# Kernel optimization log

Hardware: AMD Instinct MI355X
Metric: run time of the kernel (lower is better)

## Reference

```python
import jax, jax.numpy as jnp
import numpy as np

N = 50000          # nodes
E = 800000         # edges
F_IN, H, OUT = 512, 256, 2
BN_EPS = 1e-5


def setup_inputs() -> dict:
    key = jax.random.key(0)
    ks = jax.random.split(key, 10)
    x = jax.random.normal(ks[0], (N, F_IN), jnp.float32)
    edge_index = jax.random.randint(ks[1], (2, E), 0, N, dtype=jnp.int64)
    edge_weight = jax.random.uniform(ks[2], (E,), jnp.float32)

    def lin(k, fan_in, fan_out):
        return jax.random.normal(k, (fan_in, fan_out), jnp.float32) / np.sqrt(fan_in).astype(np.float32)

    W1, b1 = lin(ks[3], F_IN, H), jnp.zeros((H,), jnp.float32)
    W2, b2 = lin(ks[4], H, H), jnp.zeros((H,), jnp.float32)
    W3, b3 = lin(ks[5], H, OUT), jnp.zeros((OUT,), jnp.float32)
    # BatchNorm1d affine params + running stats (eval mode)
    g1, be1 = jnp.ones((H,), jnp.float32), jnp.zeros((H,), jnp.float32)
    m1 = 0.1 * jax.random.normal(ks[6], (H,), jnp.float32)
    v1 = jax.random.uniform(ks[7], (H,), jnp.float32, 0.5, 1.5)
    g2, be2 = jnp.ones((H,), jnp.float32), jnp.zeros((H,), jnp.float32)
    m2 = 0.1 * jax.random.normal(ks[8], (H,), jnp.float32)
    v2 = jax.random.uniform(ks[9], (H,), jnp.float32, 0.5, 1.5)
    return {"x": x, "edge_index": edge_index, "edge_weight": edge_weight,
            "W1": W1, "b1": b1, "g1": g1, "be1": be1, "m1": m1, "v1": v1,
            "W2": W2, "b2": b2, "g2": g2, "be2": be2, "m2": m2, "v2": v2,
            "W3": W3, "b3": b3}


def gcn_conv(x, row, col, w, W, b):
    # PyG GCNConv (eval): h = x @ W; out[col] += norm * h[row]; + b
    # row/col/w already include self-loops with weight 1.
    n = x.shape[0]
    h = x @ W                                      # [N, out]
    deg = jax.ops.segment_sum(w, col, num_segments=n)
    dinv = jnp.where(deg > 0, jax.lax.rsqrt(deg), 0.0)
    norm = dinv[row] * w * dinv[col]               # [E+N]
    out = jax.ops.segment_sum(h[row] * norm[:, None], col, num_segments=n)
    return out + b


def batchnorm_eval(x, g, be, m, v):
    return (x - m) * jax.lax.rsqrt(v + BN_EPS) * g + be


def reference(x, edge_index, edge_weight, W1, b1, g1, be1, m1, v1,
              W2, b2, g2, be2, m2, v2, W3, b3):
    n = x.shape[0]
    loops = jnp.arange(n, dtype=edge_index.dtype)
    row = jnp.concatenate([edge_index[0], loops])
    col = jnp.concatenate([edge_index[1], loops])
    w = jnp.concatenate([edge_weight, jnp.ones((n,), x.dtype)])

    h = jax.nn.relu(batchnorm_eval(gcn_conv(x, row, col, w, W1, b1), g1, be1, m1, v1))
    h = jax.nn.relu(batchnorm_eval(gcn_conv(h, row, col, w, W2, b2), g2, be2, m2, v2))
    return gcn_conv(h, row, col, w, W3, b3)
```

## Files before the change

kernel.cpp:

```cpp
#include <hip/hip_runtime.h>
#include <stdint.h>

#define F_IN 512
#define HF 256
#define OUT_F 2
#define BN_EPS 1e-5f
#define SCAN_B 256
#define LDSTR 36

typedef __attribute__((ext_vector_type(8))) short bf16x8;
typedef __attribute__((ext_vector_type(4))) float f32x4;

__device__ inline float bf2f(unsigned short u) {
    union { float f; uint32_t i; } v; v.i = ((uint32_t)u) << 16; return v.f;
}
__device__ inline unsigned short f2bf(float f) {
    union { float f; uint32_t i; } v; v.f = f;
    uint32_t r = v.i + 0x7FFFu + ((v.i >> 16) & 1u);
    return (unsigned short)(r >> 16);
}

__global__ void prep_kernel(unsigned long long* __restrict__ packed,
                            const float* __restrict__ W1, unsigned short* __restrict__ W1t,
                            const float* __restrict__ W2, unsigned short* __restrict__ W2t,
                            unsigned short* __restrict__ xbf_pad,
                            unsigned short* __restrict__ bufa_pad,
                            int n, int padx, int pada) {
    int idx = blockIdx.x * blockDim.x + threadIdx.x;
    if (idx < n) { packed[idx] = 1ULL << 20; return; }
    int j = idx - n;
    if (j < F_IN * HF) {
        int nn = j >> 9, k = j & (F_IN - 1);
        W1t[j] = f2bf(W1[(size_t)k * HF + nn]);
        return;
    }
    j -= F_IN * HF;
    if (j < HF * HF) {
        int nn = j >> 8, k = j & (HF - 1);
        W2t[j] = f2bf(W2[(size_t)k * HF + nn]);
        return;
    }
    j -= HF * HF;
    if (j < padx) { xbf_pad[j] = 0; return; }
    j -= padx;
    if (j < pada) bufa_pad[j] = 0;
}

__global__ void count_conv_kernel(const int* __restrict__ col,
                                  const float* __restrict__ w,
                                  unsigned long long* __restrict__ packed,
                                  const float* __restrict__ x,
                                  unsigned short* __restrict__ xbf,
                                  int e, int nchunk) {
    int tid = blockIdx.x * blockDim.x + threadIdx.x;
    int base = blockIdx.x * 1024 + (int)threadIdx.x;
    #pragma unroll
    for (int k = 0; k < 4; ++k) {
        int i = base + k * 256;
        if (i < e) {
            unsigned long long add = (1ULL << 40)
                | (unsigned long long)__float2uint_rn(w[i] * 1048576.0f);
            atomicAdd(&packed[col[i]], add);
        }
    }
    const int stride = gridDim.x * blockDim.x;
    const float4* x4 = (const float4*)x;
    for (int c = tid; c < nchunk; c += stride) {
        float4 f0 = x4[2 * c];
        float4 f1 = x4[2 * c + 1];
        bf16x8 v;
        v[0] = (short)f2bf(f0.x); v[1] = (short)f2bf(f0.y);
        v[2] = (short)f2bf(f0.z); v[3] = (short)f2bf(f0.w);
        v[4] = (short)f2bf(f1.x); v[5] = (short)f2bf(f1.y);
        v[6] = (short)f2bf(f1.z); v[7] = (short)f2bf(f1.w);
        *(bf16x8*)(xbf + (size_t)c * 8) = v;
    }
}

__global__ __launch_bounds__(256)
void gemm_kernel(const unsigned short* __restrict__ A,
                 const unsigned short* __restrict__ Bt,
                 unsigned short* __restrict__ C, int K) {
    __shared__ unsigned short As[2][128 * LDSTR];
    __shared__ unsigned short Bs[2][128 * LDSTR];
    const int tid  = threadIdx.x;
    const int lane = tid & 63;
    const int wv   = tid >> 6;
    const int wrow = wv >> 1, wcol = wv & 1;
    const int m0 = blockIdx.x * 128;
    const int n0 = blockIdx.y * 128;

    const int sr = tid >> 2;
    const int sc = (tid & 3) * 8;

    const unsigned short* pa0 = A + (size_t)(m0 + sr) * K + sc;
    const unsigned short* pa1 = A + (size_t)(m0 + sr + 64) * K + sc;
    const unsigned short* pb0 = Bt + (size_t)(n0 + sr) * K + sc;
    const unsigned short* pb1 = Bt + (size_t)(n0 + sr + 64) * K + sc;

    f32x4 zero4 = {0.0f, 0.0f, 0.0f, 0.0f};
    f32x4 acc[4][4];
    #pragma unroll
    for (int i = 0; i < 4; ++i)
        #pragma unroll
        for (int j = 0; j < 4; ++j) acc[i][j] = zero4;

    const int q8 = (lane >> 4) * 8;
    const int ml = lane & 15;

    bf16x8 va0 = *(const bf16x8*)pa0;
    bf16x8 va1 = *(const bf16x8*)pa1;
    bf16x8 vb0 = *(const bf16x8*)pb0;
    bf16x8 vb1 = *(const bf16x8*)pb1;

    const int nsteps = K >> 5;
    for (int s = 0; s < nsteps; ++s) {
        const int buf = s & 1;
        *(bf16x8*)&As[buf][sr * LDSTR + sc]        = va0;
        *(bf16x8*)&As[buf][(sr + 64) * LDSTR + sc] = va1;
        *(bf16x8*)&Bs[buf][sr * LDSTR + sc]        = vb0;
        *(bf16x8*)&Bs[buf][(sr + 64) * LDSTR + sc] = vb1;
        __syncthreads();
        if (s + 1 < nsteps) {
            int off = (s + 1) * 32;
            va0 = *(const bf16x8*)(pa0 + off);
            va1 = *(const bf16x8*)(pa1 + off);
            vb0 = *(const bf16x8*)(pb0 + off);
            vb1 = *(const bf16x8*)(pb1 + off);
        }
        bf16x8 af[4], bfr[4];
        #pragma unroll
        for (int i = 0; i < 4; ++i)
            af[i] = *(const bf16x8*)&As[buf][(wrow * 64 + i * 16 + ml) * LDSTR + q8];
        #pragma unroll
        for (int j = 0; j < 4; ++j)
            bfr[j] = *(const bf16x8*)&Bs[buf][(wcol * 64 + j * 16 + ml) * LDSTR + q8];
        #pragma unroll
        for (int i = 0; i < 4; ++i)
            #pragma unroll
            for (int j = 0; j < 4; ++j)
                acc[i][j] = __builtin_amdgcn_mfma_f32_16x16x32_bf16(af[i], bfr[j], acc[i][j], 0, 0, 0);
    }

    const int q4 = (lane >> 4) * 4;
    #pragma unroll
    for (int i = 0; i < 4; ++i) {
        #pragma unroll
        for (int j = 0; j < 4; ++j) {
            #pragma unroll
            for (int rg = 0; rg < 4; ++rg) {
                int r = m0 + wrow * 64 + i * 16 + q4 + rg;
                int c = n0 + wcol * 64 + j * 16 + ml;
                C[(size_t)r * HF + c] = f2bf(acc[i][j][rg]);
            }
        }
    }
}

__global__ void scan1_kernel(const unsigned long long* __restrict__ packed,
                             int* __restrict__ local, int* __restrict__ blocksum, int n) {
    __shared__ int tmp[SCAN_B];
    int i = blockIdx.x * SCAN_B + threadIdx.x;
    int v = (i < n) ? (int)(packed[i] >> 40) : 0;
    tmp[threadIdx.x] = v;
    __syncthreads();
    for (int off = 1; off < SCAN_B; off <<= 1) {
        int t = 0;
        if ((int)threadIdx.x >= off) t = tmp[threadIdx.x - off];
        __syncthreads();
        if ((int)threadIdx.x >= off) tmp[threadIdx.x] += t;
        __syncthreads();
    }
    if (i < n) local[i] = tmp[threadIdx.x] - v;
    if (threadIdx.x == SCAN_B - 1) blocksum[blockIdx.x] = tmp[SCAN_B - 1];
}

__global__ void scan3_dinv_kernel(int* __restrict__ csr_ptr, int* __restrict__ cursor,
                                  const int* __restrict__ blocksum,
                                  const unsigned long long* __restrict__ packed,
                                  float* __restrict__ dinv, int n, int e, int nb) {
    __shared__ int red[SCAN_B];
    int t = threadIdx.x;
    red[t] = (t < nb && t < (int)blockIdx.x) ? blocksum[t] : 0;
    __syncthreads();
    for (int off = SCAN_B / 2; off > 0; off >>= 1) {
        if (t < off) red[t] += red[t + off];
        __syncthreads();
    }
    int prefix = red[0];
    int i = blockIdx.x * SCAN_B + t;
    if (i < n) {
        int val = csr_ptr[i] + prefix;
        csr_ptr[i] = val;
        cursor[i] = val;
        float deg = (float)(packed[i] & 0xFFFFFFFFFFULL) * (1.0f / 1048576.0f);
        dinv[i] = rsqrtf(deg);
    }
    if (i == 0) csr_ptr[n] = e;
}

__global__ void fill_kernel(const int* __restrict__ row, const int* __restrict__ col,
                            const float* __restrict__ w, const float* __restrict__ dinv,
                            int* __restrict__ cursor, int2* __restrict__ csr_edge, int e) {
    int i = blockIdx.x * blockDim.x + threadIdx.x;
    if (i < e) {
        int r = row[i], c = col[i];
        int pos = atomicAdd(&cursor[c], 1);
        float nrm = dinv[r] * w[i] * dinv[c];
        csr_edge[pos] = make_int2(r, __float_as_int(nrm));
    }
}

template<int FINAL>
__global__ void agg_kernel(const unsigned short* __restrict__ h,
                           const int* __restrict__ ptr,
                           const int2* __restrict__ edge,
                           const float* __restrict__ dinv,
                           const float* __restrict__ b, const float* __restrict__ g,
                           const float* __restrict__ be, const float* __restrict__ m,
                           const float* __restrict__ v,
                           unsigned short* __restrict__ out,
                           const float* __restrict__ W3, float* __restrict__ h3, int n) {
    int wid  = (blockIdx.x * blockDim.x + threadIdx.x) >> 6;
    int lane = threadIdx.x & 63;
    if (wid >= n) return;
    int p0 = ptr[wid], p1 = ptr[wid + 1];
    const int fo = lane * 4;
    float a0 = 0.f, a1 = 0.f, a2 = 0.f, a3 = 0.f;

    const int pend = p0 + ((p1 - p0) & ~7);
    for (int p = p0; p < pend; p += 8) {
        int2 ed[8];
        #pragma unroll
        for (int k = 0; k < 8; ++k) ed[k] = edge[p + k];
        ushort4 hv[8];
        #pragma unroll
        for (int k = 0; k < 8; ++k)
            hv[k] = *(const ushort4*)(h + (size_t)ed[k].x * HF + fo);
        #pragma unroll
        for (int k = 0; k < 8; ++k) {
            float nw = __int_as_float(ed[k].y);
            a0 += nw * bf2f(hv[k].x);
            a1 += nw * bf2f(hv[k].y);
            a2 += nw * bf2f(hv[k].z);
            a3 += nw * bf2f(hv[k].w);
        }
    }
    if (pend < p1) {
        int2 ed[8];
        float wv[8];
        #pragma unroll
        for (int k = 0; k < 8; ++k) {
            int idx = pend + k < p1 ? pend + k : p1 - 1;
            ed[k] = edge[idx];
            wv[k] = (pend + k < p1) ? __int_as_float(ed[k].y) : 0.0f;
        }
        ushort4 hv[8];
        #pragma unroll
        for (int k = 0; k < 8; ++k)
            hv[k] = *(const ushort4*)(h + (size_t)ed[k].x * HF + fo);
        #pragma unroll
        for (int k = 0; k < 8; ++k) {
            a0 += wv[k] * bf2f(hv[k].x);
            a1 += wv[k] * bf2f(hv[k].y);
            a2 += wv[k] * bf2f(hv[k].z);
            a3 += wv[k] * bf2f(hv[k].w);
        }
    }
    float s = dinv[wid];
    float sl = s * s;
    ushort4 hv = *(const ushort4*)(h + (size_t)wid * HF + fo);
    a0 += sl * bf2f(hv.x);
    a1 += sl * bf2f(hv.y);
    a2 += sl * bf2f(hv.z);
    a3 += sl * bf2f(hv.w);

    float4 bb  = *(const float4*)(b + fo);
    float4 gg  = *(const float4*)(g + fo);
    float4 bee = *(const float4*)(be + fo);
    float4 mm  = *(const float4*)(m + fo);
    float4 vv  = *(const float4*)(v + fo);
    float f0 = fmaxf((a0 + bb.x - mm.x) * rsqrtf(vv.x + BN_EPS) * gg.x + bee.x, 0.f);
    float f1 = fmaxf((a1 + bb.y - mm.y) * rsqrtf(vv.y + BN_EPS) * gg.y + bee.y, 0.f);
    float f2 = fmaxf((a2 + bb.z - mm.z) * rsqrtf(vv.z + BN_EPS) * gg.z + bee.z, 0.f);
    float f3 = fmaxf((a3 + bb.w - mm.w) * rsqrtf(vv.w + BN_EPS) * gg.w + bee.w, 0.f);

    if (!FINAL) {
        ushort4 o;
        o.x = f2bf(f0); o.y = f2bf(f1); o.z = f2bf(f2); o.w = f2bf(f3);
        *(ushort4*)(out + (size_t)wid * HF + fo) = o;
    } else {
        float4 w0 = *(const float4*)(W3 + fo * 2);
        float4 w1 = *(const float4*)(W3 + fo * 2 + 4);
        float s0 = f0 * w0.x + f1 * w0.z + f2 * w1.x + f3 * w1.z;
        float s1 = f0 * w0.y + f1 * w0.w + f2 * w1.y + f3 * w1.w;
        #pragma unroll
        for (int o = 32; o > 0; o >>= 1) {
            s0 += __shfl_down(s0, o, 64);
            s1 += __shfl_down(s1, o, 64);
        }
        if (lane == 0) {
            h3[wid * 2 + 0] = s0;
            h3[wid * 2 + 1] = s1;
        }
    }
}

__global__ void out_kernel(const float* __restrict__ h3,
                           const int* __restrict__ ptr, const int2* __restrict__ edge,
                           const float* __restrict__ dinv,
                           const float* __restrict__ b3, float* __restrict__ out, int n) {
    int i = blockIdx.x * blockDim.x + threadIdx.x;
    if (i >= n) return;
    int p0 = ptr[i], p1 = ptr[i + 1];
    float a0 = 0.f, a1 = 0.f;
    for (int p = p0; p < p1; p += 4) {
        #pragma unroll
        for (int k = 0; k < 4; ++k) {
            int idx = p + k < p1 ? p + k : p1 - 1;
            int2 e = edge[idx];
            float nw = (p + k < p1) ? __int_as_float(e.y) : 0.0f;
            float2 u = *(const float2*)(h3 + 2 * e.x);
            a0 += nw * u.x;
            a1 += nw * u.y;
        }
    }
    float s = dinv[i];
    float sl = s * s;
    out[2 * i + 0] = a0 + sl * h3[2 * i + 0] + b3[0];
    out[2 * i + 1] = a1 + sl * h3[2 * i + 1] + b3[1];
}

static inline char* align16(char* p) {
    return (char*)(((uintptr_t)p + 15) & ~(uintptr_t)15);
}

extern "C" void kernel_launch(void* const* d_in, const int* in_sizes, int n_in,
                              void* d_out, int out_size, void* d_ws, size_t ws_size,
                              hipStream_t stream) {
    const float* x   = (const float*)d_in[0];
    const int*   ei  = (const int*)d_in[1];
    const float* ew  = (const float*)d_in[2];
    const float* W1  = (const float*)d_in[3];
    const float* b1  = (const float*)d_in[4];
    const float* g1  = (const float*)d_in[5];
    const float* be1 = (const float*)d_in[6];
    const float* m1  = (const float*)d_in[7];
    const float* v1  = (const float*)d_in[8];
    const float* W2  = (const float*)d_in[9];
    const float* b2  = (const float*)d_in[10];
    const float* g2  = (const float*)d_in[11];
    const float* be2 = (const float*)d_in[12];
    const float* m2  = (const float*)d_in[13];
    const float* v2  = (const float*)d_in[14];
    const float* W3  = (const float*)d_in[15];
    const float* b3  = (const float*)d_in[16];

    const int N  = in_sizes[0] / F_IN;
    const int E  = in_sizes[2];
    const int MP = (N + 127) & ~127;
    const int* row = ei;
    const int* col = ei + E;

    char* wsb = (char*)d_ws;
    unsigned long long* packed = (unsigned long long*)wsb; wsb = align16(wsb + (size_t)N * 8);
    float* dinv     = (float*)wsb;          wsb = align16(wsb + (size_t)N * 4);
    int*   csr_ptr  = (int*)wsb;            wsb = align16(wsb + (size_t)(N + 1) * 4);
    int*   cursor   = (int*)wsb;            wsb = align16(wsb + (size_t)N * 4);
    int*   blocksum = (int*)wsb;            wsb = align16(wsb + (size_t)SCAN_B * 4);
    int2*  csr_edge = (int2*)wsb;           wsb = align16(wsb + (size_t)E * 8);
    unsigned short* W1t = (unsigned short*)wsb;  wsb = align16(wsb + (size_t)F_IN * HF * 2);
    unsigned short* W2t = (unsigned short*)wsb;  wsb = align16(wsb + (size_t)HF * HF * 2);
    unsigned short* xbf  = (unsigned short*)wsb; wsb = align16(wsb + (size_t)MP * F_IN * 2);
    unsigned short* bufh = (unsigned short*)wsb; wsb = align16(wsb + (size_t)MP * HF * 2);
    unsigned short* bufa = (unsigned short*)wsb; wsb = align16(wsb + (size_t)MP * HF * 2);
    float* h3 = (float*)wsb;                wsb = align16(wsb + (size_t)N * OUT_F * 4);
    float* outf = (float*)d_out;

    const int TB = 256;
    const int nscan = (N + SCAN_B - 1) / SCAN_B;
    const int padx = (MP - N) * F_IN;
    const int pada = (MP - N) * HF;
    const int preptot = N + F_IN * HF + HF * HF + padx + pada;
    const int ncount = (E + 1023) / 1024;
    const int nchunk = (N * F_IN) / 8;

    prep_kernel<<<(preptot + TB - 1) / TB, TB, 0, stream>>>(
        packed, W1, W1t, W2, W2t, xbf + (size_t)N * F_IN, bufa + (size_t)N * HF, N, padx, pada);

    count_conv_kernel<<<ncount, TB, 0, stream>>>(col, ew, packed, x, xbf, E, nchunk);

    scan1_kernel<<<nscan, SCAN_B, 0, stream>>>(packed, csr_ptr, blocksum, N);
    scan3_dinv_kernel<<<nscan, SCAN_B, 0, stream>>>(csr_ptr, cursor, blocksum, packed, dinv, N, E, nscan);
    fill_kernel<<<(E + TB - 1) / TB, TB, 0, stream>>>(row, col, ew, dinv, cursor, csr_edge, E);

    dim3 ggrid(MP / 128, HF / 128);

    gemm_kernel<<<ggrid, TB, 0, stream>>>(xbf, W1t, bufh, F_IN);
    agg_kernel<0><<<((size_t)N * 64 + TB - 1) / TB, TB, 0, stream>>>(
        bufh, csr_ptr, csr_edge, dinv, b1, g1, be1, m1, v1, bufa, nullptr, nullptr, N);

    gemm_kernel<<<ggrid, TB, 0, stream>>>(bufa, W2t, bufh, HF);
    agg_kernel<1><<<((size_t)N * 64 + TB - 1) / TB, TB, 0, stream>>>(
        bufh, csr_ptr, csr_edge, dinv, b2, g2, be2, m2, v2, nullptr, W3, h3, N);

    out_kernel<<<(N + TB - 1) / TB, TB, 0, stream>>>(h3, csr_ptr, csr_edge, dinv, b3, outf, N);
}
```

Baseline: 492.5 us.

## Software-pipeline edge and feature gathers in aggregation; one edge per thread in count

The aggregation kernel now prefetches the next batch of eight gathered feature rows and the edge records two batches ahead while accumulating the current batch. The goal is to hide gather latency on the memory-bound neighbour sum. The count/convert kernel is relaunched with one edge per thread and four times as many blocks, which also spreads the x-to-bf16 conversion over more threads. Holding the extra prefetch buffers raises register pressure and may lower occupancy in the aggregation kernel.

```diff
diff --git a/kernel.cpp b/kernel.cpp
--- a/kernel.cpp
+++ b/kernel.cpp
@@ -53,15 +53,10 @@
                                   unsigned short* __restrict__ xbf,
                                   int e, int nchunk) {
     int tid = blockIdx.x * blockDim.x + threadIdx.x;
-    int base = blockIdx.x * 1024 + (int)threadIdx.x;
-    #pragma unroll
-    for (int k = 0; k < 4; ++k) {
-        int i = base + k * 256;
-        if (i < e) {
-            unsigned long long add = (1ULL << 40)
-                | (unsigned long long)__float2uint_rn(w[i] * 1048576.0f);
-            atomicAdd(&packed[col[i]], add);
-        }
+    if (tid < e) {
+        unsigned long long add = (1ULL << 40)
+            | (unsigned long long)__float2uint_rn(w[tid] * 1048576.0f);
+        atomicAdd(&packed[col[tid]], add);
     }
     const int stride = gridDim.x * blockDim.x;
     const float4* x4 = (const float4*)x;
@@ -228,24 +223,49 @@
     const int fo = lane * 4;
     float a0 = 0.f, a1 = 0.f, a2 = 0.f, a3 = 0.f;
 
-    const int pend = p0 + ((p1 - p0) & ~7);
-    for (int p = p0; p < pend; p += 8) {
-        int2 ed[8];
-        #pragma unroll
-        for (int k = 0; k < 8; ++k) ed[k] = edge[p + k];
-        ushort4 hv[8];
+    const int cnt = p1 - p0;
+    const int nb  = cnt >> 3;
+
+    int2 edC[8], edN[8];
+    ushort4 hvC[8];
+
+    if (nb > 0) {
+        #pragma unroll
+        for (int k = 0; k < 8; ++k) edC[k] = edge[p0 + k];
+        if (nb > 1) {
+            #pragma unroll
+            for (int k = 0; k < 8; ++k) edN[k] = edge[p0 + 8 + k];
+        }
         #pragma unroll
         for (int k = 0; k < 8; ++k)
-            hv[k] = *(const ushort4*)(h + (size_t)ed[k].x * HF + fo);
-        #pragma unroll
-        for (int k = 0; k < 8; ++k) {
-            float nw = __int_as_float(ed[k].y);
-            a0 += nw * bf2f(hv[k].x);
-            a1 += nw * bf2f(hv[k].y);
-            a2 += nw * bf2f(hv[k].z);
-            a3 += nw * bf2f(hv[k].w);
-        }
-    }
+            hvC[k] = *(const ushort4*)(h + (size_t)edC[k].x * HF + fo);
+
+        for (int bb = 0; bb < nb; ++bb) {
+            ushort4 hvN[8];
+            int2 edN2[8];
+            if (bb + 1 < nb) {
+                if (bb + 2 < nb) {
+                    int pp = p0 + (bb + 2) * 8;
+                    #pragma unroll
+                    for (int k = 0; k < 8; ++k) edN2[k] = edge[pp + k];
+                }
+                #pragma unroll
+                for (int k = 0; k < 8; ++k)
+                    hvN[k] = *(const ushort4*)(h + (size_t)edN[k].x * HF + fo);
+            }
+            #pragma unroll
+            for (int k = 0; k < 8; ++k) {
+                float nw = __int_as_float(edC[k].y);
+                a0 += nw * bf2f(hvC[k].x);
+                a1 += nw * bf2f(hvC[k].y);
+                a2 += nw * bf2f(hvC[k].z);
+                a3 += nw * bf2f(hvC[k].w);
+            }
+            #pragma unroll
+            for (int k = 0; k < 8; ++k) { edC[k] = edN[k]; edN[k] = edN2[k]; hvC[k] = hvN[k]; }
+        }
+    }
+    const int pend = p0 + nb * 8;
     if (pend < p1) {
         int2 ed[8];
         float wv[8];
@@ -382,13 +402,13 @@
     const int padx = (MP - N) * F_IN;
     const int pada = (MP - N) * HF;
     const int preptot = N + F_IN * HF + HF * HF + padx + pada;
-    const int ncount = (E + 1023) / 1024;
+    const int ncc = (E + TB - 1) / TB;
     const int nchunk = (N * F_IN) / 8;
 
     prep_kernel<<<(preptot + TB - 1) / TB, TB, 0, stream>>>(
         packed, W1, W1t, W2, W2t, xbf + (size_t)N * F_IN, bufa + (size_t)N * HF, N, padx, pada);
 
-    count_conv_kernel<<<ncount, TB, 0, stream>>>(col, ew, packed, x, xbf, E, nchunk);
+    count_conv_kernel<<<ncc, TB, 0, stream>>>(col, ew, packed, x, xbf, E, nchunk);
 
     scan1_kernel<<<nscan, SCAN_B, 0, stream>>>(packed, csr_ptr, blocksum, N);
     scan3_dinv_kernel<<<nscan, SCAN_B, 0, stream>>>(csr_ptr, cursor, blocksum, packed, dinv, N, E, nscan);
```

After: 471.1 us. 4.3% less time.
